# Kernel optimization log

Hardware: AMD Instinct MI355X
Metric: run time of the kernel (lower is better)

## Reference

```python
import jax, jax.numpy as jnp
import numpy as np

B, T, D, H = 2, 2048, 1024, 16
DH = D // H
PD = 6
SCALE = DH ** -0.5
_PAIRS4 = [(0, 1), (0, 2), (0, 3), (1, 2), (1, 3), (2, 3)]
_J6 = jnp.array([[0, 0, 0, 0, 0, 1], [0, 0, 0, 0, -1, 0], [0, 0, 0, 1, 0, 0],
                 [0, 0, 1, 0, 0, 0], [0, -1, 0, 0, 0, 0], [1, 0, 0, 0, 0, 0]], dtype=jnp.float32)


def exterior(p1, p2):
    # p1, p2: (..., 4) -> normalized 6-d Plucker line (..., 6)
    parts = [p1[..., i] * p2[..., j] - p1[..., j] * p2[..., i] for i, j in _PAIRS4]
    L = jnp.stack(parts, axis=-1)
    n = jnp.linalg.norm(L, axis=-1, keepdims=True)
    return L / jnp.clip(n, 1e-12)


def setup_inputs() -> dict:
    key = jax.random.key(0)
    ks = jax.random.split(key, 12)
    s = 0.02
    return {
        'x': jax.random.normal(ks[0], (B, T, D), jnp.float32),
        'qkv_w': jax.random.normal(ks[1], (D, 3 * D), jnp.float32) * s,
        'qkv_b': jnp.zeros((3 * D,), jnp.float32),
        'w1_write': jax.random.normal(ks[2], (D, 4 * H), jnp.float32) * s,
        'w2_write': jax.random.normal(ks[3], (D, 4 * H), jnp.float32) * s,
        'w1_read': jax.random.normal(ks[4], (D, 4 * H), jnp.float32) * s,
        'w2_read': jax.random.normal(ks[5], (D, 4 * H), jnp.float32) * s,
        'memv_w': jax.random.normal(ks[6], (D, D), jnp.float32) * s,
        'memv_b': jnp.zeros((D,), jnp.float32),
        'memg_w': jax.random.normal(ks[7], (D, H), jnp.float32) * s,
        'memg_b': jnp.zeros((H,), jnp.float32),
        'mem_scale': jnp.full((H,), 0.1, jnp.float32),
        'rw_mix': jnp.zeros((), jnp.float32),
        'out_w': jax.random.normal(ks[8], (D, D), jnp.float32) * s,
        'out_b': jnp.zeros((D,), jnp.float32),
        'decay_logits': jnp.full((H,), 4.6, jnp.float32),
    }


def reference(x, qkv_w, qkv_b, w1_write, w2_write, w1_read, w2_read,
              memv_w, memv_b, memg_w, memg_b, mem_scale, rw_mix,
              out_w, out_b, decay_logits):
    # ---- standard causal softmax attention ----
    qkv = (x @ qkv_w + qkv_b).reshape(B, T, 3, H, DH).transpose(2, 0, 3, 1, 4)
    q, k, v = qkv[0], qkv[1], qkv[2]                      # each (B,H,T,DH)
    scores = jnp.einsum('bhtd,bhsd->bhts', q, k) * SCALE
    mask = jnp.triu(jnp.ones((T, T), bool), 1)
    scores = jnp.where(mask[None, None], -jnp.inf, scores)
    attn = jax.nn.softmax(scores, axis=-1)                # dropout=0 (eval)
    seq_out = jnp.einsum('bhts,bhsd->bthd', attn, v).reshape(B, T, D)

    # ---- Plucker lines for write (prev->cur) and read ----
    x_prev = jnp.concatenate([jnp.zeros((B, 1, D), x.dtype), x[:, :-1]], axis=1)
    w1 = (x_prev @ w1_write).reshape(B, T, H, 4)
    w2 = (x @ w2_write).reshape(B, T, H, 4)
    write_lines = exterior(w1, w2)                        # (B,T,H,6)
    r1 = (x @ w1_read).reshape(B, T, H, 4)
    r2 = (x @ w2_read).reshape(B, T, H, 4)
    read_lines = exterior(r1, r2)

    Jw = jnp.einsum('bthi,ij->bhtj', write_lines, _J6)    # (B,H,T,6)
    Jr = jnp.einsum('bthi,ij->bhtj', read_lines, _J6)
    rd = read_lines.transpose(0, 2, 1, 3)                 # (B,H,T,6)

    # ---- decay-weighted cumsum of 6x6 outer-product states ----
    decays = jax.nn.sigmoid(decay_logits)                 # (H,)
    pos = jnp.arange(T, dtype=x.dtype)
    decay_inv = (1.0 / jnp.clip(decays, 1e-6))[:, None] ** pos[None]   # (H,T)
    decay_fwd = decays[:, None] ** pos[None]                           # (H,T)

    def shifted_state(Jv):
        outer = Jv[..., :, None] * Jv[..., None, :]       # (B,H,T,6,6)
        ow = outer * decay_inv[None, :, :, None, None]
        M = jnp.cumsum(ow, axis=2)
        M = jnp.concatenate([jnp.zeros((B, H, 1, PD, PD), x.dtype), M[:, :, :-1]], axis=2)
        return M * decay_fwd[None, :, :, None, None]

    Mw = shifted_state(Jw)
    Mr = shifted_state(Jr)

    score_w = jnp.einsum('bhti,bhtij,bhtj->bht', rd, Mw, rd)
    score_r = jnp.einsum('bhti,bhtij,bhtj->bht', Jw, Mr, Jw)
    alpha = jax.nn.sigmoid(rw_mix)
    mem_score = (1 - alpha) * score_w + alpha * score_r   # (B,H,T)

    mem_val = x @ memv_w + memv_b                         # (B,T,D)
    gate = jax.nn.sigmoid(x @ memg_w + memg_b)            # (B,T,H)
    mem_score_t = mem_score.transpose(0, 2, 1)            # (B,T,H)
    gated = jax.nn.sigmoid(mem_score_t * mem_scale[None, None, :]) * gate
    gated = gated.mean(axis=-1, keepdims=True)            # (B,T,1)

    return (seq_out + gated * mem_val) @ out_w + out_b
```

## Files before the change

kernel.cpp:

```cpp
#include <hip/hip_runtime.h>

#define Bb 2
#define Tt 2048
#define Dd 1024
#define Hh 16
#define LDC 4480

typedef __attribute__((ext_vector_type(8))) short s16x8;
typedef __attribute__((ext_vector_type(4))) float f32x4;
typedef __attribute__((ext_vector_type(8))) _Float16 f16x8;

__device__ __forceinline__ float bf2f(unsigned short u) {
  unsigned v = ((unsigned)u) << 16;
  union { unsigned u; float f; } c; c.u = v; return c.f;
}
__device__ __forceinline__ unsigned short f2bf(float f) {
  union { float f; unsigned u; } c; c.f = f;
  unsigned u = c.u + 0x7fffu + ((c.u >> 16) & 1u);
  return (unsigned short)(u >> 16);
}
__device__ __forceinline__ float sigm(float x) { return 1.f / (1.f + expf(-x)); }



__global__ __launch_bounds__(256) void prep_kernel(const float* __restrict__ x,
                                                   const float* __restrict__ qkv_w,
                                                   const float* __restrict__ w1w,
                                                   const float* __restrict__ w2w,
                                                   const float* __restrict__ w1r,
                                                   const float* __restrict__ w2r,
                                                   const float* __restrict__ memg_w,
                                                   const float* __restrict__ memv_w,
                                                   const float* __restrict__ out_w,
                                                   const float* __restrict__ qkv_b,
                                                   const float* __restrict__ memg_b,
                                                   const float* __restrict__ memv_b,
                                                   unsigned short* __restrict__ xb,
                                                   unsigned short* __restrict__ WT,
                                                   unsigned short* __restrict__ outT,
                                                   float* __restrict__ biasC) {
  __shared__ float tile[32][33];
  int id = blockIdx.x;
  if (id < 2048) {
    int i = id * 256 + threadIdx.x;
    int row = i >> 7;
    int k8 = i & 127;
    const float4* xv = reinterpret_cast<const float4*>(x + (size_t)i * 8);
    float4 a = xv[0], b = xv[1];
    s16x8 out;
    out[0] = (short)f2bf(a.x); out[1] = (short)f2bf(a.y);
    out[2] = (short)f2bf(a.z); out[3] = (short)f2bf(a.w);
    out[4] = (short)f2bf(b.x); out[5] = (short)f2bf(b.y);
    out[6] = (short)f2bf(b.z); out[7] = (short)f2bf(b.w);
    int mt = row >> 4, kt = k8 >> 2, quad = k8 & 3;
    int lane = (row & 15) + quad * 16;
    *(s16x8*)&xb[(((size_t)mt * 32 + kt) * 64 + lane) * 8] = out;
  } else if (id < 6528) {
    int j = id - 2048;
    int n0 = (j % 140) * 32, kt = j / 140, k0 = kt * 32;
    int tx = threadIdx.x & 31, ty = threadIdx.x >> 5;
#pragma unroll
    for (int i = 0; i < 4; i++) {
      int k = k0 + ty + i * 8, n = n0 + tx;
      float v;
      if (n < 3072)       v = qkv_w[(size_t)k * 3072 + n];
      else if (n < 3136)  v = w1w[k * 64 + (n - 3072)];
      else if (n < 3200)  v = w2w[k * 64 + (n - 3136)];
      else if (n < 3264)  v = w1r[k * 64 + (n - 3200)];
      else if (n < 3328)  v = w2r[k * 64 + (n - 3264)];
      else if (n < 3344)  v = memg_w[k * 16 + (n - 3328)];
      else if (n < 3392)  v = 0.f;
      else if (n < 4416)  v = memv_w[(size_t)k * 1024 + (n - 3392)];
      else                v = 0.f;
      tile[ty + i * 8][tx] = v;
    }
    __syncthreads();
    if (threadIdx.x < 128) {
      int nl = threadIdx.x & 31, quad = threadIdx.x >> 5;
      s16x8 out;
#pragma unroll
      for (int e = 0; e < 8; e++) out[e] = (short)f2bf(tile[quad * 8 + e][nl]);
      int nt = (n0 >> 4) + (nl >> 4);
      int lane = (nl & 15) + quad * 16;
      *(s16x8*)&WT[(((size_t)nt * 32 + kt) * 64 + lane) * 8] = out;
    }
  } else if (id < 7552) {
    int j = id - 6528;
    int n0 = (j & 31) * 32, kt = j >> 5, k0 = kt * 32;
    int tx = threadIdx.x & 31, ty = threadIdx.x >> 5;
#pragma unroll
    for (int i = 0; i < 4; i++) {
      int k = k0 + ty + i * 8, n = n0 + tx;
      tile[ty + i * 8][tx] = out_w[(size_t)k * 1024 + n];
    }
    __syncthreads();
    if (threadIdx.x < 128) {
      int nl = threadIdx.x & 31, quad = threadIdx.x >> 5;
      s16x8 out;
#pragma unroll
      for (int e = 0; e < 8; e++) out[e] = (short)f2bf(tile[quad * 8 + e][nl]);
      int nt = (n0 >> 4) + (nl >> 4);
      int lane = (nl & 15) + quad * 16;
      *(s16x8*)&outT[(((size_t)nt * 32 + kt) * 64 + lane) * 8] = out;
    }
  } else {
    int i = (id - 7552) * 256 + threadIdx.x;
    if (i < LDC) {
      float v = 0.f;
      if (i < 3072) v = qkv_b[i];
      else if (i >= 3328 && i < 3344) v = memg_b[i - 3328];
      else if (i >= 3392 && i < 4416) v = memv_b[i - 3392];
      biasC[i] = v;
    }
  }
}


template <int MODE>
__global__ __launch_bounds__(256) void gemm_frag_kernel(const unsigned short* __restrict__ Af,
                                                        const unsigned short* __restrict__ Bf,
                                                        void* __restrict__ Cout,
                                                        const float* __restrict__ bias) {
  int mTile, nTile;
  if (MODE == 0) {
    const int xx = blockIdx.x & 7, local = blockIdx.x >> 3;
    mTile = (xx >> 1) * 8 + (local & 7);
    nTile = (xx & 1) * 18 + (local >> 3);
    if (nTile >= 35) return;
  } else {
    mTile = blockIdx.x >> 3;
    nTile = blockIdx.x & 7;
  }
  const int lane = threadIdx.x & 63, wid = threadIdx.x >> 6;
  const int quad = lane >> 4, c16 = lane & 15;
  const int wm = wid >> 1, wn = wid & 1;
  const int mt0 = mTile * 8 + wm * 4;
  const int nt0 = nTile * 8 + wn * 4;
  const unsigned short* Apt = Af + ((size_t)mt0 * 32 * 64 + lane) * 8;
  const unsigned short* Bpt = Bf + ((size_t)nt0 * 32 * 64 + lane) * 8;

  f32x4 acc[4][4] = {};
  s16x8 af[2][4], bf[2][4];
#pragma unroll
  for (int i = 0; i < 4; i++) {
    af[0][i] = *(const s16x8*)(Apt + (size_t)i * 16384);
    bf[0][i] = *(const s16x8*)(Bpt + (size_t)i * 16384);
  }
#pragma unroll
  for (int kt = 0; kt < 32; kt++) {
    const int cur = kt & 1, nxt = cur ^ 1;
    if (kt + 1 < 32) {
      const unsigned short* An = Apt + (size_t)(kt + 1) * 512;
      const unsigned short* Bn = Bpt + (size_t)(kt + 1) * 512;
#pragma unroll
      for (int i = 0; i < 4; i++) {
        af[nxt][i] = *(const s16x8*)(An + (size_t)i * 16384);
        bf[nxt][i] = *(const s16x8*)(Bn + (size_t)i * 16384);
      }
    }
#pragma unroll
    for (int mt = 0; mt < 4; mt++)
#pragma unroll
      for (int nt = 0; nt < 4; nt++)
        acc[mt][nt] = __builtin_amdgcn_mfma_f32_16x16x32_bf16(af[cur][mt], bf[cur][nt],
                                                              acc[mt][nt], 0, 0, 0);
  }

#pragma unroll
  for (int mt = 0; mt < 4; mt++)
#pragma unroll
    for (int nt = 0; nt < 4; nt++) {
      int col = (nt0 + nt) * 16 + c16;
      float bv = bias[col];
#pragma unroll
      for (int r = 0; r < 4; r++) {
        int row = (mt0 + mt) * 16 + quad * 4 + r;
        if (MODE == 0)
          ((unsigned short*)Cout)[(size_t)row * 4480 + col] = f2bf(acc[mt][nt][r] + bv);
        else
          ((float*)Cout)[(size_t)row * 1024 + col] = acc[mt][nt][r] + bv;
      }
    }
}


__device__ __forceinline__ void ext6(const float* p, const float* q, float* L) {
  L[0] = p[0] * q[1] - p[1] * q[0];
  L[1] = p[0] * q[2] - p[2] * q[0];
  L[2] = p[0] * q[3] - p[3] * q[0];
  L[3] = p[1] * q[2] - p[2] * q[1];
  L[4] = p[1] * q[3] - p[3] * q[1];
  L[5] = p[2] * q[3] - p[3] * q[2];
  float n = sqrtf(L[0]*L[0] + L[1]*L[1] + L[2]*L[2] + L[3]*L[3] + L[4]*L[4] + L[5]*L[5]);
  float inv = 1.f / fmaxf(n, 1e-12f);
#pragma unroll
  for (int k = 0; k < 6; k++) L[k] *= inv;
}


__global__ __launch_bounds__(256) void post1_kernel(const unsigned short* __restrict__ Cq,
                                                    unsigned short* __restrict__ Kt,
                                                    unsigned short* __restrict__ Vt,
                                                    float* __restrict__ Jw,
                                                    float* __restrict__ Jr,
                                                    float* __restrict__ rd) {
  __shared__ unsigned short vt[32 * 66];
  int id = blockIdx.x;
  int tid = threadIdx.x;
  if (id < 2048) {
    int kb = id & 63, bh = id >> 6;
    int b = bh >> 4, h = bh & 15;
    size_t tbase = ((size_t)bh * 64 + kb) * 2048;
    {
      int key = tid >> 3, p = tid & 7, dg = p ^ (key & 7);
      size_t src = (size_t)(b * Tt + kb * 32 + key) * LDC + 1024 + h * 64 + dg * 8;
      s16x8 kv = *(const s16x8*)&Cq[src];
      *(s16x8*)&Kt[tbase + (size_t)tid * 8] = kv;
    }
    {
      int row = tid >> 3, c = tid & 7;
      size_t src = (size_t)(b * Tt + kb * 32 + row) * LDC + 2048 + h * 64 + c * 8;
      s16x8 vv = *(const s16x8*)&Cq[src];
#pragma unroll
      for (int e = 0; e < 8; e++) {
        union { _Float16 hf; unsigned short s; } cv;
        cv.hf = (_Float16)bf2f((unsigned short)vv[e]);
        vt[row * 66 + c * 8 + e] = cv.s;
      }
    }
    __syncthreads();
    {
      int d = tid >> 2, p = tid & 3, cq = p ^ ((d >> 2) & 3);
      s16x8 out;
#pragma unroll
      for (int e = 0; e < 8; e++) {
        int key = ((e >> 2) & 1) * 16 + cq * 4 + (e & 3);
        out[e] = (short)vt[key * 66 + d];
      }
      *(s16x8*)&Vt[tbase + (size_t)tid * 8] = out;
    }
  } else {
    int idx = (id - 2048) * 256 + tid;
    int h = idx & 15, t = (idx >> 4) & 2047, b = idx >> 15;
    size_t row = (size_t)(b * Tt + t) * LDC;
    float w1[4], w2[4], r1[4], r2[4];
#pragma unroll
    for (int k = 0; k < 4; k++) {
      w1[k] = (t > 0) ? bf2f(Cq[row - LDC + 3072 + h * 4 + k]) : 0.f;
      w2[k] = bf2f(Cq[row + 3136 + h * 4 + k]);
      r1[k] = bf2f(Cq[row + 3200 + h * 4 + k]);
      r2[k] = bf2f(Cq[row + 3264 + h * 4 + k]);
    }
    float Lw[6], Lr[6];
    ext6(w1, w2, Lw);
    ext6(r1, r2, Lr);
    size_t ob = ((size_t)(b * Hh + h) * Tt + t) * 6;
    Jw[ob + 0] = Lw[5]; Jw[ob + 1] = -Lw[4]; Jw[ob + 2] = Lw[3];
    Jw[ob + 3] = Lw[2]; Jw[ob + 4] = -Lw[1]; Jw[ob + 5] = Lw[0];
    Jr[ob + 0] = Lr[5]; Jr[ob + 1] = -Lr[4]; Jr[ob + 2] = Lr[3];
    Jr[ob + 3] = Lr[2]; Jr[ob + 4] = -Lr[1]; Jr[ob + 5] = Lr[0];
#pragma unroll
    for (int k = 0; k < 6; k++) rd[ob + k] = Lr[k];
  }
}


__device__ __forceinline__ void do_tile(int ks, int q0, int quad, int c16,
                                        const s16x8& qf0, const s16x8& qf1,
                                        const s16x8 kf[2][2], const f16x8 vb[4],
                                        float& l_i, f32x4 o[4]) {
  f32x4 st0 = {}, st1 = {};
  st0 = __builtin_amdgcn_mfma_f32_16x16x32_bf16(kf[0][0], qf0, st0, 0, 0, 0);
  st0 = __builtin_amdgcn_mfma_f32_16x16x32_bf16(kf[0][1], qf1, st0, 0, 0, 0);
  st1 = __builtin_amdgcn_mfma_f32_16x16x32_bf16(kf[1][0], qf0, st1, 0, 0, 0);
  st1 = __builtin_amdgcn_mfma_f32_16x16x32_bf16(kf[1][1], qf1, st1, 0, 0, 0);
  bool need_mask = (ks + 31 > q0);
  f16x8 pa;
  float lp = 0.f;
#pragma unroll
  for (int r = 0; r < 4; r++) {
    float v0 = st0[r] * 0.125f;
    float v1 = st1[r] * 0.125f;
    if (need_mask) {
      v0 = (ks + quad * 4 + r      <= q0 + c16) ? v0 : -1e30f;
      v1 = (ks + 16 + quad * 4 + r <= q0 + c16) ? v1 : -1e30f;
    }
    float p0 = __expf(v0);
    float p1 = __expf(v1);
    lp += p0 + p1;
    pa[r]     = (_Float16)p0;
    pa[4 + r] = (_Float16)p1;
  }
  l_i += lp;
#pragma unroll
  for (int nt = 0; nt < 4; nt++)
    o[nt] = __builtin_amdgcn_mfma_f32_16x16x32_f16(pa, vb[nt], o[nt], 0, 0, 0);
}

__global__ __launch_bounds__(256) void attn_kernel(const unsigned short* __restrict__ Cq,
                                                   const unsigned short* __restrict__ Kt,
                                                   const unsigned short* __restrict__ Vt,
                                                   unsigned short* __restrict__ po) {
  __shared__ unsigned short Kl[2048];
  __shared__ unsigned short Vl[2048];
  const int g0 = blockIdx.x, bh = blockIdx.y;
  const int g = ((bh >> 4) & 1) ? (15 - g0) : g0;
  const int b = bh >> 4, h = bh & 15;
  const int w = threadIdx.x >> 6, lane = threadIdx.x & 63;
  const int quad = lane >> 4, c16 = lane & 15;
  const int pi = g * 4 + w;
  const int qA = pi * 16, qB = 2032 - pi * 16;
  const int nkA = qA + 16, nkB = 2048 - pi * 16;
  const int bound = 2048 - 64 * g;
  const unsigned short* Ktb = Kt + (size_t)bh * 64 * 2048;
  const unsigned short* Vtb = Vt + (size_t)bh * 64 * 2048;
  const int ci = threadIdx.x;

  size_t rowA = (size_t)(b * Tt + qA + c16) * LDC + h * 64;
  size_t rowB = (size_t)(b * Tt + qB + c16) * LDC + h * 64;
  s16x8 qA0 = *(const s16x8*)&Cq[rowA + quad * 8];
  s16x8 qA1 = *(const s16x8*)&Cq[rowA + 32 + quad * 8];
  s16x8 qB0 = *(const s16x8*)&Cq[rowB + quad * 8];
  s16x8 qB1 = *(const s16x8*)&Cq[rowB + 32 + quad * 8];

  float lA = 0.f, lB = 0.f;
  f32x4 oA[4] = {}, oB[4] = {};

  {
    s16x8 k0 = *(const s16x8*)&Ktb[(size_t)ci * 8];
    s16x8 v0 = *(const s16x8*)&Vtb[(size_t)ci * 8];
    *(s16x8*)&Kl[ci * 8] = k0;
    *(s16x8*)&Vl[ci * 8] = v0;
  }
  __syncthreads();

  for (int ks = 0; ks < bound; ks += 32) {
    bool more = (ks + 32) < bound;
    s16x8 kreg, vreg;
    if (more) {
      size_t nb = ((size_t)(ks >> 5) + 1) * 2048 + (size_t)ci * 8;
      kreg = *(const s16x8*)&Ktb[nb];
      vreg = *(const s16x8*)&Vtb[nb];
    }
    if (ks < nkB) {
      s16x8 kf[2][2];
#pragma unroll
      for (int gg = 0; gg < 2; gg++)
#pragma unroll
        for (int half = 0; half < 2; half++) {
          int key = gg * 16 + c16;
          int p = (half * 4 + quad) ^ (c16 & 7);
          kf[gg][half] = *(const s16x8*)&Kl[(key * 8 + p) * 8];
        }
      f16x8 vb[4];
#pragma unroll
      for (int nt = 0; nt < 4; nt++) {
        int d = nt * 16 + c16;
        int p = quad ^ ((d >> 2) & 3);
        vb[nt] = *(const f16x8*)&Vl[(d * 4 + p) * 8];
      }
      do_tile(ks, qB, quad, c16, qB0, qB1, kf, vb, lB, oB);
      if (ks < nkA)
        do_tile(ks, qA, quad, c16, qA0, qA1, kf, vb, lA, oA);
    }
    __syncthreads();
    if (more) {
      *(s16x8*)&Kl[ci * 8] = kreg;
      *(s16x8*)&Vl[ci * 8] = vreg;
      __syncthreads();
    }
  }

  lB += __shfl_xor(lB, 16, 64); lB += __shfl_xor(lB, 32, 64);
  lA += __shfl_xor(lA, 16, 64); lA += __shfl_xor(lA, 32, 64);
  float invB = 1.f / lB, invA = 1.f / lA;
#pragma unroll
  for (int r = 0; r < 4; r++) {
    float ivB = __shfl(invB, quad * 4 + r, 64);
    float ivA = __shfl(invA, quad * 4 + r, 64);
    size_t baseB = (size_t)(b * Tt + qB + quad * 4 + r) * Dd + h * 64;
    size_t baseA = (size_t)(b * Tt + qA + quad * 4 + r) * Dd + h * 64;
#pragma unroll
    for (int nt = 0; nt < 4; nt++) {
      po[baseB + nt * 16 + c16] = f2bf(oB[nt][r] * ivB);
      po[baseA + nt * 16 + c16] = f2bf(oA[nt][r] * ivA);
    }
  }
}


__global__ __launch_bounds__(64) void scanA_kernel(const float* __restrict__ Jw,
                                                   const float* __restrict__ Jr,
                                                   const float* __restrict__ decay_logits,
                                                   float* __restrict__ chunkA) {
  int blk = blockIdx.x;
  int chunk = blk & 15, bh = (blk >> 4) & 31, type = blk >> 9;
  int lane = threadIdx.x;
  const float* V = (type == 0 ? Jw : Jr) + ((size_t)bh * Tt + chunk * 128) * 6;
  __shared__ float v[768];
  for (int i = lane; i < 768; i += 64) v[i] = V[i];
  __syncthreads();
  float d = sigm(decay_logits[bh & 15]);
  int ll = lane < 36 ? lane : 35;
  int i6 = ll / 6, j6 = ll % 6;
  float A = 0.f;
  for (int s = 0; s < 128; s++) A = d * A + v[s * 6 + i6] * v[s * 6 + j6];
  if (lane < 36) chunkA[((size_t)(type * 32 + bh) * 16 + chunk) * 36 + lane] = A;
}


__global__ __launch_bounds__(128) void scanB_kernel(const float* __restrict__ Jw,
                                                    const float* __restrict__ Jr,
                                                    const float* __restrict__ rd,
                                                    const float* __restrict__ chunkA,
                                                    const float* __restrict__ decay_logits,
                                                    float* __restrict__ score_w,
                                                    float* __restrict__ score_r) {
  int blk = blockIdx.x;
  int chunk = blk & 15, bh = (blk >> 4) & 31, type = blk >> 9;
  int tl = threadIdx.x;
  size_t tb = ((size_t)bh * Tt + chunk * 128) * 6;
  const float* U = (type == 0 ? rd : Jw) + tb;
  const float* W = (type == 0 ? Jw : Jr) + tb;
  __shared__ float wv[768];
  __shared__ float Bm[36];
  for (int i = tl; i < 768; i += 128) wv[i] = W[i];
  float d = sigm(decay_logits[bh & 15]);
  if (tl < 36) {
    float dS = powf(d, 128.f);
    float Bv = 0.f;
    size_t base = (size_t)(type * 32 + bh) * 16;
    for (int c = 0; c < chunk; c++)
      Bv = dS * Bv + d * chunkA[(base + c) * 36 + tl];
    Bm[tl] = Bv;
  }
  __syncthreads();
  float u[6];
#pragma unroll
  for (int i = 0; i < 6; i++) u[i] = U[tl * 6 + i];
  float q = 0.f;
#pragma unroll
  for (int i = 0; i < 6; i++) {
    float bi = 0.f;
#pragma unroll
    for (int j = 0; j < 6; j++) bi += Bm[i * 6 + j] * u[j];
    q += u[i] * bi;
  }
  float acc = 0.f;
  for (int s = 0; s < tl; s++) {
    const float* ws = &wv[s * 6];
    float dot = u[0]*ws[0] + u[1]*ws[1] + u[2]*ws[2] + u[3]*ws[3] + u[4]*ws[4] + u[5]*ws[5];
    acc = d * (acc + dot * dot);
  }
  float score = acc + powf(d, (float)tl) * q;
  float* outp = (type == 0 ? score_w : score_r);
  outp[(size_t)bh * Tt + chunk * 128 + tl] = score;
}


__global__ __launch_bounds__(256) void combine_kernel(const unsigned short* __restrict__ po,
                                                      const unsigned short* __restrict__ Cq,
                                                      const float* __restrict__ score_w,
                                                      const float* __restrict__ score_r,
                                                      const float* __restrict__ mem_scale,
                                                      const float* __restrict__ rw_mix,
                                                      unsigned short* __restrict__ fused) {
  __shared__ float tmp[16];
  int rowi = blockIdx.x;
  int b = rowi >> 11, t = rowi & 2047;
  float alpha = sigm(rw_mix[0]);
  if (threadIdx.x < 16) {
    int h = threadIdx.x;
    size_t sh = (size_t)(b * 16 + h) * Tt + t;
    float ms = (1.f - alpha) * score_w[sh] + alpha * score_r[sh];
    float gate = sigm(bf2f(Cq[(size_t)rowi * LDC + 3328 + h]));
    tmp[h] = sigm(ms * mem_scale[h]) * gate;
  }
  __syncthreads();
  float g = 0.f;
#pragma unroll
  for (int h = 0; h < 16; h++) g += tmp[h];
  g *= (1.f / 16.f);
  if (threadIdx.x < 128) {
    int c = threadIdx.x;
    int d0 = c * 8;
    s16x8 ov = *(const s16x8*)&po[((size_t)b * Tt + t) * Dd + d0];
    s16x8 mv = *(const s16x8*)&Cq[(size_t)rowi * LDC + 3392 + d0];
    s16x8 out;
#pragma unroll
    for (int e = 0; e < 8; e++)
      out[e] = (short)f2bf(bf2f((unsigned short)ov[e]) + g * bf2f((unsigned short)mv[e]));
    int mt = rowi >> 4, kt = c >> 2, quad = c & 3;
    int lane = (rowi & 15) + quad * 16;
    *(s16x8*)&fused[(((size_t)mt * 32 + kt) * 64 + lane) * 8] = out;
  }
}


extern "C" void kernel_launch(void* const* d_in, const int* in_sizes, int n_in,
                              void* d_out, int out_size, void* d_ws, size_t ws_size,
                              hipStream_t stream) {
  (void)in_sizes; (void)n_in; (void)out_size; (void)ws_size;
  const float* x         = (const float*)d_in[0];
  const float* qkv_w     = (const float*)d_in[1];
  const float* qkv_b     = (const float*)d_in[2];
  const float* w1w       = (const float*)d_in[3];
  const float* w2w       = (const float*)d_in[4];
  const float* w1r       = (const float*)d_in[5];
  const float* w2r       = (const float*)d_in[6];
  const float* memv_w    = (const float*)d_in[7];
  const float* memv_b    = (const float*)d_in[8];
  const float* memg_w    = (const float*)d_in[9];
  const float* memg_b    = (const float*)d_in[10];
  const float* mem_scale = (const float*)d_in[11];
  const float* rw_mix    = (const float*)d_in[12];
  const float* out_w     = (const float*)d_in[13];
  const float* out_b     = (const float*)d_in[14];
  const float* decay_l   = (const float*)d_in[15];

  char* w = (char*)d_ws;
  unsigned short* xb    = (unsigned short*)(w + 0);
  unsigned short* Kt    = (unsigned short*)(w + 0);
  unsigned short* WT    = (unsigned short*)(w + 8388608);
  unsigned short* Vt    = (unsigned short*)(w + 8388608);
  unsigned short* outT  = (unsigned short*)(w + 17563648);
  float*          biasC = (float*)(w + 19660800);
  unsigned short* Cbuf  = (unsigned short*)(w + 19678720);
  unsigned short* po    = (unsigned short*)(w + 56378880);
  float*          Jw    = (float*)(w + 73680384);
  float*          Jr    = (float*)(w + 75253248);
  float*          rd    = (float*)(w + 76826112);
  float*          chA   = (float*)(w + 78398976);
  float*          sw    = (float*)(w + 78693888);
  float*          sr    = (float*)(w + 78956032);
  unsigned short* fused = (unsigned short*)(w + 79218176);

  prep_kernel<<<7570, 256, 0, stream>>>(x, qkv_w, w1w, w2w, w1r, w2r, memg_w, memv_w,
                                        out_w, qkv_b, memg_b, memv_b,
                                        xb, WT, outT, biasC);

  gemm_frag_kernel<0><<<1152, 256, 0, stream>>>(xb, WT, Cbuf, biasC);

  post1_kernel<<<2304, 256, 0, stream>>>(Cbuf, Kt, Vt, Jw, Jr, rd);
  attn_kernel<<<dim3(16, 32), 256, 0, stream>>>(Cbuf, Kt, Vt, po);
  scanA_kernel<<<1024, 64, 0, stream>>>(Jw, Jr, decay_l, chA);
  scanB_kernel<<<1024, 128, 0, stream>>>(Jw, Jr, rd, chA, decay_l, sw, sr);
  combine_kernel<<<4096, 256, 0, stream>>>(po, Cbuf, sw, sr, mem_scale, rw_mix, fused);

  gemm_frag_kernel<1><<<256, 256, 0, stream>>>(fused, outT, d_out, out_b);
}
```

Baseline: 279.7 us.

## Load attention K/V fragments directly from global with register double-buffering

Replaces the shared-memory staging of K/V tiles, with its two block barriers per step, by per-wave direct global loads into MFMA fragment registers, ping-ponging two register tile sets. Each wave now loops only to its own key bound instead of the block-wide bound. The grid is flattened to 1D with an XCD-aware mapping so that blocks of the same head land on the same XCD for L2 reuse, and MFMA sections are wrapped in s_setprio. The cost is more global and L2 traffic, since each wave reads K/V itself with no cross-wave sharing, plus higher register pressure. The g reversal used for load balancing is also dropped.

```diff
diff --git a/kernel.cpp b/kernel.cpp
--- a/kernel.cpp
+++ b/kernel.cpp
@@ -270,10 +270,12 @@
                                         const s16x8 kf[2][2], const f16x8 vb[4],
                                         float& l_i, f32x4 o[4]) {
   f32x4 st0 = {}, st1 = {};
+  __builtin_amdgcn_s_setprio(1);
   st0 = __builtin_amdgcn_mfma_f32_16x16x32_bf16(kf[0][0], qf0, st0, 0, 0, 0);
   st0 = __builtin_amdgcn_mfma_f32_16x16x32_bf16(kf[0][1], qf1, st0, 0, 0, 0);
   st1 = __builtin_amdgcn_mfma_f32_16x16x32_bf16(kf[1][0], qf0, st1, 0, 0, 0);
   st1 = __builtin_amdgcn_mfma_f32_16x16x32_bf16(kf[1][1], qf1, st1, 0, 0, 0);
+  __builtin_amdgcn_s_setprio(0);
   bool need_mask = (ks + 31 > q0);
   f16x8 pa;
   float lp = 0.f;
@@ -292,29 +294,32 @@
     pa[4 + r] = (_Float16)p1;
   }
   l_i += lp;
+  __builtin_amdgcn_s_setprio(1);
 #pragma unroll
   for (int nt = 0; nt < 4; nt++)
     o[nt] = __builtin_amdgcn_mfma_f32_16x16x32_f16(pa, vb[nt], o[nt], 0, 0, 0);
+  __builtin_amdgcn_s_setprio(0);
 }
 
 __global__ __launch_bounds__(256) void attn_kernel(const unsigned short* __restrict__ Cq,
                                                    const unsigned short* __restrict__ Kt,
                                                    const unsigned short* __restrict__ Vt,
                                                    unsigned short* __restrict__ po) {
-  __shared__ unsigned short Kl[2048];
-  __shared__ unsigned short Vl[2048];
-  const int g0 = blockIdx.x, bh = blockIdx.y;
-  const int g = ((bh >> 4) & 1) ? (15 - g0) : g0;
+  const int id = blockIdx.x;
+  const int xcd = id & 7, rest = id >> 3;
+  const int g = rest & 15;
+  const int bh = ((rest >> 4) << 3) | xcd;
   const int b = bh >> 4, h = bh & 15;
   const int w = threadIdx.x >> 6, lane = threadIdx.x & 63;
   const int quad = lane >> 4, c16 = lane & 15;
   const int pi = g * 4 + w;
   const int qA = pi * 16, qB = 2032 - pi * 16;
   const int nkA = qA + 16, nkB = 2048 - pi * 16;
-  const int bound = 2048 - 64 * g;
-  const unsigned short* Ktb = Kt + (size_t)bh * 64 * 2048;
-  const unsigned short* Vtb = Vt + (size_t)bh * 64 * 2048;
-  const int ci = threadIdx.x;
+  const char* Kbase = (const char*)(Kt + (size_t)bh * 64 * 2048);
+  const char* Vbase = (const char*)(Vt + (size_t)bh * 64 * 2048);
+  const int vK0 = c16 * 128 + ((quad       ^ (c16 & 7)) * 16);
+  const int vK1 = c16 * 128 + (((4 + quad) ^ (c16 & 7)) * 16);
+  const int vV  = c16 * 64  + ((quad ^ ((c16 >> 2) & 3)) * 16);
 
   size_t rowA = (size_t)(b * Tt + qA + c16) * LDC + h * 64;
   size_t rowB = (size_t)(b * Tt + qB + c16) * LDC + h * 64;
@@ -326,50 +331,36 @@
   float lA = 0.f, lB = 0.f;
   f32x4 oA[4] = {}, oB[4] = {};
 
-  {
-    s16x8 k0 = *(const s16x8*)&Ktb[(size_t)ci * 8];
-    s16x8 v0 = *(const s16x8*)&Vtb[(size_t)ci * 8];
-    *(s16x8*)&Kl[ci * 8] = k0;
-    *(s16x8*)&Vl[ci * 8] = v0;
-  }
-  __syncthreads();
-
-  for (int ks = 0; ks < bound; ks += 32) {
-    bool more = (ks + 32) < bound;
-    s16x8 kreg, vreg;
-    if (more) {
-      size_t nb = ((size_t)(ks >> 5) + 1) * 2048 + (size_t)ci * 8;
-      kreg = *(const s16x8*)&Ktb[nb];
-      vreg = *(const s16x8*)&Vtb[nb];
-    }
-    if (ks < nkB) {
-      s16x8 kf[2][2];
-#pragma unroll
-      for (int gg = 0; gg < 2; gg++)
-#pragma unroll
-        for (int half = 0; half < 2; half++) {
-          int key = gg * 16 + c16;
-          int p = (half * 4 + quad) ^ (c16 & 7);
-          kf[gg][half] = *(const s16x8*)&Kl[(key * 8 + p) * 8];
-        }
-      f16x8 vb[4];
-#pragma unroll
-      for (int nt = 0; nt < 4; nt++) {
-        int d = nt * 16 + c16;
-        int p = quad ^ ((d >> 2) & 3);
-        vb[nt] = *(const f16x8*)&Vl[(d * 4 + p) * 8];
-      }
-      do_tile(ks, qB, quad, c16, qB0, qB1, kf, vb, lB, oB);
-      if (ks < nkA)
-        do_tile(ks, qA, quad, c16, qA0, qA1, kf, vb, lA, oA);
-    }
-    __syncthreads();
-    if (more) {
-      *(s16x8*)&Kl[ci * 8] = kreg;
-      *(s16x8*)&Vl[ci * 8] = vreg;
-      __syncthreads();
-    }
-  }
+  s16x8 kfX[2][2], kfY[2][2];
+  f16x8 vbX[4], vbY[4];
+
+#define LOADT(dstK, dstV, kb) do {                                   \
+    const char* Kb_ = Kbase + (size_t)(kb) * 4096;                   \
+    const char* Vb_ = Vbase + (size_t)(kb) * 4096;                   \
+    dstK[0][0] = *(const s16x8*)(Kb_ + vK0);                         \
+    dstK[0][1] = *(const s16x8*)(Kb_ + vK1);                         \
+    dstK[1][0] = *(const s16x8*)(Kb_ + 2048 + vK0);                  \
+    dstK[1][1] = *(const s16x8*)(Kb_ + 2048 + vK1);                  \
+    dstV[0] = *(const f16x8*)(Vb_ + vV);                             \
+    dstV[1] = *(const f16x8*)(Vb_ + 1024 + vV);                      \
+    dstV[2] = *(const f16x8*)(Vb_ + 2048 + vV);                      \
+    dstV[3] = *(const f16x8*)(Vb_ + 3072 + vV);                      \
+  } while (0)
+
+  LOADT(kfX, vbX, 0);
+  for (int ks = 0; ks < nkB; ks += 64) {
+    if (ks + 32 < nkB) LOADT(kfY, vbY, (ks >> 5) + 1);
+    do_tile(ks, qB, quad, c16, qB0, qB1, kfX, vbX, lB, oB);
+    if (ks < nkA)
+      do_tile(ks, qA, quad, c16, qA0, qA1, kfX, vbX, lA, oA);
+    if (ks + 32 < nkB) {
+      if (ks + 64 < nkB) LOADT(kfX, vbX, (ks >> 5) + 2);
+      do_tile(ks + 32, qB, quad, c16, qB0, qB1, kfY, vbY, lB, oB);
+      if (ks + 32 < nkA)
+        do_tile(ks + 32, qA, quad, c16, qA0, qA1, kfY, vbY, lA, oA);
+    }
+  }
+#undef LOADT
 
   lB += __shfl_xor(lB, 16, 64); lB += __shfl_xor(lB, 32, 64);
   lA += __shfl_xor(lA, 16, 64); lA += __shfl_xor(lA, 32, 64);
@@ -542,7 +533,7 @@
   gemm_frag_kernel<0><<<1152, 256, 0, stream>>>(xb, WT, Cbuf, biasC);
 
   post1_kernel<<<2304, 256, 0, stream>>>(Cbuf, Kt, Vt, Jw, Jr, rd);
-  attn_kernel<<<dim3(16, 32), 256, 0, stream>>>(Cbuf, Kt, Vt, po);
+  attn_kernel<<<512, 256, 0, stream>>>(Cbuf, Kt, Vt, po);
   scanA_kernel<<<1024, 64, 0, stream>>>(Jw, Jr, decay_l, chA);
   scanB_kernel<<<1024, 128, 0, stream>>>(Jw, Jr, rd, chA, decay_l, sw, sr);
   combine_kernel<<<4096, 256, 0, stream>>>(po, Cbuf, sw, sr, mem_scale, rw_mix, fused);
```

Result: faster. 270.1 us (-3.4%).
